# Kernel optimization log

Measured on AMD Instinct MI355X. Metric: run time of the kernel, lower is better.

The kernel has to match this reference:

```python
import jax, jax.numpy as jnp
import numpy as np

NUM_HEADS = 8


def _ln(x, w, b, eps=1e-5):
    mu = x.mean(-1, keepdims=True)
    var = ((x - mu) ** 2).mean(-1, keepdims=True)
    return (x - mu) * jax.lax.rsqrt(var + eps) * w + b


def _qkv(x, w, H, d):
    # x: (n, l, C) -> q,k,v each (n, H, l, d)
    n, l, _ = x.shape
    qkv = (x @ w.T).reshape(n, l, 3, H, d)
    qkv = jnp.transpose(qkv, (2, 0, 3, 1, 4))
    return qkv[0], qkv[1], qkv[2]


def _qkv_head(x, w, d):
    # x: (n, H, l, d) -> q,k,v each (n, H, l, d); linear acts on head_dim
    n, H, l, _ = x.shape
    qkv = (x @ w.T).reshape(n, H, l, 3, d)
    qkv = jnp.transpose(qkv, (3, 0, 1, 2, 4))
    return qkv[0], qkv[1], qkv[2]


def _attn(q, k, v, scale):
    s = jax.nn.softmax(jnp.einsum('nhqd,nhkd->nhqk', q, k) * scale, axis=-1)
    return jnp.einsum('nhqk,nhkd->nhqd', s, v)


def setup_inputs() -> dict:
    key = jax.random.key(0)
    ks = jax.random.split(key, 10)
    B, N, C = 16, 4096, 512
    l = 64
    H, d = NUM_HEADS, C // NUM_HEADS
    return {
        'x': jax.random.normal(ks[0], (B, N, C), jnp.float32),
        'n3_w': jnp.ones((C,), jnp.float32),
        'n3_b': jnp.zeros((C,), jnp.float32),
        'n4_w': jnp.ones((C,), jnp.float32),
        'n4_b': jnp.zeros((C,), jnp.float32),
        'ln1_w': jax.random.normal(ks[1], (3 * C, C), jnp.float32) * 0.02,
        'ln2_w': jax.random.normal(ks[2], (3 * C, C), jnp.float32) * 0.02,
        'ln3_w': jax.random.normal(ks[3], (3 * d, d), jnp.float32) * 0.02,
        'ln4_w': jax.random.normal(ks[4], (3 * d, d), jnp.float32) * 0.02,
        'pos1': jax.random.normal(ks[5], (1, l, C), jnp.float32),
        'pos2': jax.random.normal(ks[6], (1, l, C), jnp.float32),
        'pos3': jax.random.normal(ks[7], (1, H, l, d), jnp.float32),
        'pos4': jax.random.normal(ks[8], (1, H, l, d), jnp.float32),
    }


def reference(x, n3_w, n3_b, n4_w, n4_b, ln1_w, ln2_w, ln3_w, ln4_w,
              pos1, pos2, pos3, pos4):
    B, N, C = x.shape
    l = int(np.sqrt(N))
    H = NUM_HEADS
    d = C // H
    scale = d ** -0.5

    # window (row) branch
    x_w = _ln(x, n3_w, n3_b).reshape(B * l, l, C) + pos1
    q, k, v = _qkv(x_w, ln1_w, H, d)
    x_ww = _attn(q, k, v, scale) + pos3                     # (B*l, H, l, d)
    xw_q, xw_k, xw_v = _qkv_head(x_ww, ln3_w, d)

    # height (column) branch: transpose the l x l grid
    x_h = _ln(x, n4_w, n4_b).reshape(B, l, l, C)
    x_h = jnp.swapaxes(x_h, 1, 2).reshape(B * l, l, C) + pos2
    q, k, v = _qkv(x_h, ln2_w, H, d)
    x_hh = _attn(q, k, v, scale) + pos4
    xh_q, xh_k, xh_v = _qkv_head(x_hh, ln4_w, d)

    # cross-attention between the two axial branches
    o1 = _attn(xh_q, xw_k, xw_v, scale)                     # (B*l, H, l, d)
    o1 = jnp.swapaxes(o1, 1, 2).reshape(B, l, l, C)
    o1 = jnp.swapaxes(o1, 1, 2)
    o2 = _attn(xw_q, xh_k, xh_v, scale)
    o2 = jnp.swapaxes(o2, 1, 2).reshape(B, l, l, C)

    out = (o1 + o2).reshape(B, N, C) + x
    return out
```

## Files before the change

kernel.cpp:

```cpp
#include <hip/hip_runtime.h>

typedef unsigned short u16;
typedef __attribute__((ext_vector_type(8))) short bf16x8;
typedef __attribute__((ext_vector_type(4))) float floatx4;
typedef __attribute__((ext_vector_type(4))) unsigned short u16x4;

__device__ __forceinline__ float b2f(u16 u) {
  unsigned int i = ((unsigned int)u) << 16;
  return __builtin_bit_cast(float, i);
}
__device__ __forceinline__ u16 f2b(float f) {
  unsigned int i = __builtin_bit_cast(unsigned int, f);
  i += 0x7fffu + ((i >> 16) & 1u);
  return (u16)(i >> 16);
}
#define MFMA16(a, b, c) __builtin_amdgcn_mfma_f32_16x16x32_bf16((a), (b), (c), 0, 0, 0)
#define LGKM0() __asm__ volatile("s_waitcnt lgkmcnt(0)" ::: "memory")

__device__ __forceinline__ void gload_lds16(const u16* g, u16* l) {
  __builtin_amdgcn_global_load_lds(
      (const __attribute__((address_space(1))) void*)g,
      (__attribute__((address_space(3))) void*)l, 16, 0, 0);
}

__global__ __launch_bounds__(256) void cvt_kernel(const float* __restrict__ a,
                                                  u16* __restrict__ o, int n4) {
  int i = blockIdx.x * 256 + threadIdx.x;
  if (i < n4) {
    float4 v = ((const float4*)a)[i];
    u16x4 r;
    r.x = f2b(v.x); r.y = f2b(v.y); r.z = f2b(v.z); r.w = f2b(v.w);
    ((u16x4*)o)[i] = r;
  }
}

__global__ __launch_bounds__(256) void ln_pos_kernel(
    const float* __restrict__ x, const float* __restrict__ n3w, const float* __restrict__ n3b,
    const float* __restrict__ n4w, const float* __restrict__ n4b,
    const float* __restrict__ pos1, const float* __restrict__ pos2,
    u16* __restrict__ yW, u16* __restrict__ yH) {
  int wv = threadIdx.x >> 6, lane = threadIdx.x & 63;
  int token = blockIdx.x * 4 + wv;
  int b = token >> 12, r = (token >> 6) & 63, c = token & 63;
  const float4* xr = (const float4*)(x + (size_t)token * 512) + lane * 2;
  float4 x0 = xr[0], x1 = xr[1];
  float v[8] = {x0.x, x0.y, x0.z, x0.w, x1.x, x1.y, x1.z, x1.w};
  float s = 0.f, ss = 0.f;
#pragma unroll
  for (int j = 0; j < 8; j++) { s += v[j]; ss += v[j] * v[j]; }
#pragma unroll
  for (int off = 1; off < 64; off <<= 1) { s += __shfl_xor(s, off); ss += __shfl_xor(ss, off); }
  float mu = s * (1.0f / 512.0f);
  float var = ss * (1.0f / 512.0f) - mu * mu;
  float rs = rsqrtf(var + 1e-5f);
  int ch0 = lane * 8;
  float w3[8], b3[8], w4[8], b4[8], p1[8], p2[8];
  *(float4*)&w3[0] = *(const float4*)(n3w + ch0); *(float4*)&w3[4] = *(const float4*)(n3w + ch0 + 4);
  *(float4*)&b3[0] = *(const float4*)(n3b + ch0); *(float4*)&b3[4] = *(const float4*)(n3b + ch0 + 4);
  *(float4*)&w4[0] = *(const float4*)(n4w + ch0); *(float4*)&w4[4] = *(const float4*)(n4w + ch0 + 4);
  *(float4*)&b4[0] = *(const float4*)(n4b + ch0); *(float4*)&b4[4] = *(const float4*)(n4b + ch0 + 4);
  const float* p1p = pos1 + (size_t)c * 512 + ch0;
  const float* p2p = pos2 + (size_t)r * 512 + ch0;
  *(float4*)&p1[0] = *(const float4*)p1p; *(float4*)&p1[4] = *(const float4*)(p1p + 4);
  *(float4*)&p2[0] = *(const float4*)p2p; *(float4*)&p2[4] = *(const float4*)(p2p + 4);
  bf16x8 ow, oh;
#pragma unroll
  for (int j = 0; j < 8; j++) {
    float xn = (v[j] - mu) * rs;
    ow[j] = (short)f2b(xn * w3[j] + b3[j] + p1[j]);
    oh[j] = (short)f2b(xn * w4[j] + b4[j] + p2[j]);
  }
  *(bf16x8*)(yW + (size_t)token * 512 + ch0) = ow;
  size_t hrow = (size_t)b * 4096 + (size_t)c * 64 + r;
  *(bf16x8*)(yH + hrow * 512 + ch0) = oh;
}

__global__ __launch_bounds__(256) void qkv_gemm_kernel(
    const u16* __restrict__ A0, const u16* __restrict__ A1,
    const u16* __restrict__ W0, const u16* __restrict__ W1,
    u16* __restrict__ Z0, u16* __restrict__ Z1) {
  const int K = 512, N = 1536;
  int br = blockIdx.z;
  const u16* A = br ? A1 : A0;
  const u16* W = br ? W1 : W0;
  u16* Z = br ? Z1 : Z0;
  int n0 = blockIdx.x * 128, m0 = blockIdx.y * 128;
  __shared__ u16 gpool[8192];
  u16 (*As)[32] = (u16(*)[32])gpool;
  u16 (*Bs)[32] = (u16(*)[32])(gpool + 4096);
  int tid = threadIdx.x, lane = tid & 63, wave = tid >> 6;
  int wm = (wave >> 1) * 64, wn = (wave & 1) * 64;
  int ml = lane & 15, quad = lane >> 4;
  floatx4 acc[4][4];
#pragma unroll
  for (int mi = 0; mi < 4; mi++)
#pragma unroll
    for (int ni = 0; ni < 4; ni++) acc[mi][ni] = (floatx4){0.f, 0.f, 0.f, 0.f};

  int srow = (lane >> 2);
  int scol = (lane & 3) * 8;
  for (int kt = 0; kt < K; kt += 32) {
#pragma unroll
    for (int i = 0; i < 2; i++) {
      int rbase = wave * 32 + i * 16;
      gload_lds16(A + (size_t)(m0 + rbase + srow) * K + kt + scol, &As[rbase][0]);
      gload_lds16(W + (size_t)(n0 + rbase + srow) * K + kt + scol, &Bs[rbase][0]);
    }
    __syncthreads();
    bf16x8 a[4], bfr[4];
#pragma unroll
    for (int mi = 0; mi < 4; mi++) a[mi] = *(const bf16x8*)&As[wm + mi * 16 + ml][quad * 8];
#pragma unroll
    for (int ni = 0; ni < 4; ni++) bfr[ni] = *(const bf16x8*)&Bs[wn + ni * 16 + ml][quad * 8];
#pragma unroll
    for (int mi = 0; mi < 4; mi++)
#pragma unroll
      for (int ni = 0; ni < 4; ni++) acc[mi][ni] = MFMA16(a[mi], bfr[ni], acc[mi][ni]);
    __syncthreads();
  }
  u16* wl = gpool + wave * 2048;
#pragma unroll
  for (int pair = 0; pair < 2; pair++) {
#pragma unroll
    for (int mh = 0; mh < 2; mh++) {
      int mi = pair * 2 + mh;
#pragma unroll
      for (int ni = 0; ni < 4; ni++)
#pragma unroll
        for (int r = 0; r < 4; r++)
          wl[(mh * 16 + quad * 4 + r) * 64 + ni * 16 + ml] = f2b(acc[mi][ni][r]);
    }
    LGKM0();
#pragma unroll
    for (int p = 0; p < 4; p++) {
      int lrow = p * 8 + (lane >> 3);
      int col8 = (lane & 7) * 8;
      bf16x8 vv = *(const bf16x8*)&wl[lrow * 64 + col8];
      int rg = m0 + wm + pair * 32 + lrow;
      *(bf16x8*)&Z[(size_t)rg * N + n0 + wn + col8] = vv;
    }
    LGKM0();
  }
}

__device__ __forceinline__ void attn_core(bf16x8 aq0, bf16x8 aq1,
                                          const u16 (*Ks)[72], const u16 (*Vt)[72],
                                          u16 (*Psw)[72], int lane, floatx4 o[4]) {
  int ml = lane & 15, quad = lane >> 4;
  floatx4 s[4];
#pragma unroll
  for (int nt = 0; nt < 4; nt++) {
    floatx4 z = (floatx4){0.f, 0.f, 0.f, 0.f};
    bf16x8 b0 = *(const bf16x8*)&Ks[nt * 16 + ml][quad * 8];
    bf16x8 b1 = *(const bf16x8*)&Ks[nt * 16 + ml][32 + quad * 8];
    z = MFMA16(aq0, b0, z);
    z = MFMA16(aq1, b1, z);
    s[nt] = z;
  }
#pragma unroll
  for (int r = 0; r < 4; r++) {
    float m = -1e30f;
#pragma unroll
    for (int nt = 0; nt < 4; nt++) { s[nt][r] *= 0.125f; m = fmaxf(m, s[nt][r]); }
#pragma unroll
    for (int off = 1; off < 16; off <<= 1) m = fmaxf(m, __shfl_xor(m, off));
    float su = 0.f;
#pragma unroll
    for (int nt = 0; nt < 4; nt++) { float p = __expf(s[nt][r] - m); s[nt][r] = p; su += p; }
#pragma unroll
    for (int off = 1; off < 16; off <<= 1) su += __shfl_xor(su, off);
    float inv = 1.0f / su;
#pragma unroll
    for (int nt = 0; nt < 4; nt++) s[nt][r] *= inv;
  }
#pragma unroll
  for (int nt = 0; nt < 4; nt++)
#pragma unroll
    for (int r = 0; r < 4; r++) Psw[quad * 4 + r][nt * 16 + ml] = f2b(s[nt][r]);
  LGKM0();
  bf16x8 ap0 = *(const bf16x8*)&Psw[ml][quad * 8];
  bf16x8 ap1 = *(const bf16x8*)&Psw[ml][32 + quad * 8];
#pragma unroll
  for (int et = 0; et < 4; et++) {
    floatx4 z = (floatx4){0.f, 0.f, 0.f, 0.f};
    bf16x8 b0 = *(const bf16x8*)&Vt[et * 16 + ml][quad * 8];
    bf16x8 b1 = *(const bf16x8*)&Vt[et * 16 + ml][32 + quad * 8];
    z = MFMA16(ap0, b0, z);
    z = MFMA16(ap1, b1, z);
    o[et] = z;
  }
}

__device__ __forceinline__ void head_qkv(const floatx4 o[4], const float* pp,
                                         const u16* lw, u16 (*Ks)[72], u16 (*Vt)[72],
                                         u16 (*Ps)[72], int wv, int lane,
                                         bf16x8& axq0, bf16x8& axq1) {
  int ml = lane & 15, quad = lane >> 4;
#pragma unroll
  for (int et = 0; et < 4; et++)
#pragma unroll
    for (int r = 0; r < 4; r++) {
      int qp = wv * 16 + quad * 4 + r, e = et * 16 + ml;
      Ps[quad * 4 + r][et * 16 + ml] = f2b(o[et][r] + pp[(size_t)qp * 64 + e]);
    }
  LGKM0();
  bf16x8 ax0 = *(const bf16x8*)&Ps[ml][quad * 8];
  bf16x8 ax1 = *(const bf16x8*)&Ps[ml][32 + quad * 8];
  LGKM0();
  __builtin_amdgcn_sched_barrier(0);
#pragma unroll
  for (int nj = 0; nj < 4; nj++) {
    int col = 64 + nj * 16 + ml;
    bf16x8 b0 = *(const bf16x8*)(lw + (size_t)col * 64 + quad * 8);
    bf16x8 b1 = *(const bf16x8*)(lw + (size_t)col * 64 + 32 + quad * 8);
    floatx4 z = (floatx4){0.f, 0.f, 0.f, 0.f};
    z = MFMA16(ax0, b0, z);
    z = MFMA16(ax1, b1, z);
#pragma unroll
    for (int r = 0; r < 4; r++)
      Ks[wv * 16 + quad * 4 + r][nj * 16 + ml] = f2b(z[r]);
  }
#pragma unroll
  for (int nj = 0; nj < 4; nj++) {
    int col = 128 + nj * 16 + ml;
    bf16x8 b0 = *(const bf16x8*)(lw + (size_t)col * 64 + quad * 8);
    bf16x8 b1 = *(const bf16x8*)(lw + (size_t)col * 64 + 32 + quad * 8);
    floatx4 z = (floatx4){0.f, 0.f, 0.f, 0.f};
    z = MFMA16(ax0, b0, z);
    z = MFMA16(ax1, b1, z);
#pragma unroll
    for (int r = 0; r < 4; r++)
      Vt[nj * 16 + ml][wv * 16 + quad * 4 + r] = f2b(z[r]);
  }
#pragma unroll
  for (int nj = 0; nj < 4; nj++) {
    int col = nj * 16 + ml;
    bf16x8 b0 = *(const bf16x8*)(lw + (size_t)col * 64 + quad * 8);
    bf16x8 b1 = *(const bf16x8*)(lw + (size_t)col * 64 + 32 + quad * 8);
    floatx4 z = (floatx4){0.f, 0.f, 0.f, 0.f};
    z = MFMA16(ax0, b0, z);
    z = MFMA16(ax1, b1, z);
#pragma unroll
    for (int r = 0; r < 4; r++)
      Ps[quad * 4 + r][nj * 16 + ml] = f2b(z[r]);
  }
  LGKM0();
  __builtin_amdgcn_sched_barrier(0);
  axq0 = *(const bf16x8*)&Ps[ml][quad * 8];
  axq1 = *(const bf16x8*)&Ps[ml][32 + quad * 8];
  LGKM0();
}

__global__ __launch_bounds__(256) void fused_attn_kernel(
    const u16* __restrict__ Zw, const u16* __restrict__ Zh,
    const u16* __restrict__ l3b, const u16* __restrict__ l4b,
    const float* __restrict__ pos3, const float* __restrict__ pos4,
    u16* __restrict__ o1b, u16* __restrict__ o2b) {
  int w = blockIdx.x, h = blockIdx.y;
  __shared__ u16 pool[23040];
  u16 (*KsW)[72] = (u16(*)[72])pool;
  u16 (*VtW)[72] = (u16(*)[72])(pool + 4608);
  u16 (*KsH)[72] = (u16(*)[72])(pool + 9216);
  u16 (*VtH)[72] = (u16(*)[72])(pool + 13824);
  int tid = threadIdx.x, lane = tid & 63, wv = tid >> 6;
  int ml = lane & 15, quad = lane >> 4;
  u16 (*Ps)[72] = (u16(*)[72])(pool + 18432 + wv * 1152);
  const u16* baseW = Zw + (size_t)w * 64 * 1536 + h * 64;
  const u16* baseH = Zh + (size_t)w * 64 * 1536 + h * 64;
  for (int i = tid; i < 512; i += 256) {
    int r = i >> 3, c = (i & 7) * 8;
    *(bf16x8*)&KsW[r][c] = *(const bf16x8*)(baseW + 512 + (size_t)r * 1536 + c);
    *(bf16x8*)&KsH[r][c] = *(const bf16x8*)(baseH + 512 + (size_t)r * 1536 + c);
  }
  for (int i = tid; i < 1024; i += 256) {
    int p = i >> 4, e0 = (i & 15) * 4;
    u16x4 vW = *(const u16x4*)(baseW + 1024 + (size_t)p * 1536 + e0);
    u16x4 vH = *(const u16x4*)(baseH + 1024 + (size_t)p * 1536 + e0);
    VtW[e0 + 0][p] = vW.x; VtW[e0 + 1][p] = vW.y; VtW[e0 + 2][p] = vW.z; VtW[e0 + 3][p] = vW.w;
    VtH[e0 + 0][p] = vH.x; VtH[e0 + 1][p] = vH.y; VtH[e0 + 2][p] = vH.z; VtH[e0 + 3][p] = vH.w;
  }
  const u16* qrW = baseW + (size_t)(wv * 16 + ml) * 1536 + quad * 8;
  const u16* qrH = baseH + (size_t)(wv * 16 + ml) * 1536 + quad * 8;
  bf16x8 aqW0 = *(const bf16x8*)qrW;
  bf16x8 aqW1 = *(const bf16x8*)(qrW + 32);
  bf16x8 aqH0 = *(const bf16x8*)qrH;
  bf16x8 aqH1 = *(const bf16x8*)(qrH + 32);
  __syncthreads();
  floatx4 oW[4], oH[4];
  attn_core(aqW0, aqW1, KsW, VtW, Ps, lane, oW);
  attn_core(aqH0, aqH1, KsH, VtH, Ps, lane, oH);
  __syncthreads();
  bf16x8 axqW0, axqW1, axqH0, axqH1;
  head_qkv(oW, pos3 + (size_t)h * 4096, l3b, KsW, VtW, Ps, wv, lane, axqW0, axqW1);
  __syncthreads();
  head_qkv(oH, pos4 + (size_t)h * 4096, l4b, KsH, VtH, Ps, wv, lane, axqH0, axqH1);
  __syncthreads();
  floatx4 c2[4], c1[4];
  attn_core(axqW0, axqW1, KsH, VtH, Ps, lane, c2);
  attn_core(axqH0, axqH1, KsW, VtW, Ps, lane, c1);
  __syncthreads();
  u16* Out1 = pool;
  u16* Out2 = pool + 4608;
#pragma unroll
  for (int et = 0; et < 4; et++)
#pragma unroll
    for (int r = 0; r < 4; r++) {
      int row = wv * 16 + quad * 4 + r;
      Out1[row * 64 + et * 16 + ml] = f2b(c1[et][r]);
      Out2[row * 64 + et * 16 + ml] = f2b(c2[et][r]);
    }
  __syncthreads();
  u16* o1p = o1b + (size_t)w * 32768 + h * 64;
  u16* o2p = o2b + (size_t)w * 32768 + h * 64;
#pragma unroll
  for (int j = 0; j < 2; j++) {
    int c = tid + j * 256;
    int pos = c >> 3, cc = (c & 7) * 8;
    *(bf16x8*)&o1p[(size_t)pos * 512 + cc] = *(const bf16x8*)&Out1[pos * 64 + cc];
    *(bf16x8*)&o2p[(size_t)pos * 512 + cc] = *(const bf16x8*)&Out2[pos * 64 + cc];
  }
}

__global__ __launch_bounds__(256) void final_add_kernel(
    const float* __restrict__ x, const u16* __restrict__ o1b,
    const u16* __restrict__ o2b, float* __restrict__ out) {
  int wv = threadIdx.x >> 6, lane = threadIdx.x & 63;
  int token = blockIdx.x * 4 + wv;
  int b = token >> 12, r = (token >> 6) & 63, c = token & 63;
  size_t i = (size_t)token * 512 + lane * 8;
  size_t i1 = ((size_t)b * 4096 + (size_t)c * 64 + r) * 512 + lane * 8;
  float vx[8];
  *(float4*)&vx[0] = *(const float4*)(x + i);
  *(float4*)&vx[4] = *(const float4*)(x + i + 4);
  bf16x8 v1 = *(const bf16x8*)(o1b + i1);
  bf16x8 v2 = *(const bf16x8*)(o2b + i);
  float vo[8];
#pragma unroll
  for (int j = 0; j < 8; j++)
    vo[j] = vx[j] + b2f((u16)v1[j]) + b2f((u16)v2[j]);
  *(float4*)(out + i) = *(float4*)&vo[0];
  *(float4*)(out + i + 4) = *(float4*)&vo[4];
}

extern "C" void kernel_launch(void* const* d_in, const int* in_sizes, int n_in,
                              void* d_out, int out_size, void* d_ws, size_t ws_size,
                              hipStream_t stream) {
  const float* x    = (const float*)d_in[0];
  const float* n3w  = (const float*)d_in[1];
  const float* n3b  = (const float*)d_in[2];
  const float* n4w  = (const float*)d_in[3];
  const float* n4b  = (const float*)d_in[4];
  const float* ln1  = (const float*)d_in[5];
  const float* ln2  = (const float*)d_in[6];
  const float* ln3  = (const float*)d_in[7];
  const float* ln4  = (const float*)d_in[8];
  const float* pos1 = (const float*)d_in[9];
  const float* pos2 = (const float*)d_in[10];
  const float* pos3 = (const float*)d_in[11];
  const float* pos4 = (const float*)d_in[12];

  char* ws = (char*)d_ws;
  u16* yW = (u16*)ws;
  u16* yH = (u16*)(ws + (size_t)67108864);
  u16* Zw = (u16*)(ws + (size_t)134217728);
  u16* Zh = (u16*)(ws + (size_t)335544320);
  u16* o1b = yW;
  u16* o2b = yH;
  float* out = (float*)d_out;

  u16* Wb1 = (u16*)d_out;
  u16* Wb2 = Wb1 + 786432;
  u16* l3b = Wb2 + 786432;
  u16* l4b = l3b + 12288;

  cvt_kernel<<<768, 256, 0, stream>>>(ln1, Wb1, 196608);
  cvt_kernel<<<768, 256, 0, stream>>>(ln2, Wb2, 196608);
  cvt_kernel<<<12, 256, 0, stream>>>(ln3, l3b, 3072);
  cvt_kernel<<<12, 256, 0, stream>>>(ln4, l4b, 3072);
  ln_pos_kernel<<<16384, 256, 0, stream>>>(x, n3w, n3b, n4w, n4b, pos1, pos2, yW, yH);
  qkv_gemm_kernel<<<dim3(12, 512, 2), 256, 0, stream>>>(yW, yH, Wb1, Wb2, Zw, Zh);
  fused_attn_kernel<<<dim3(1024, 8), 256, 0, stream>>>(Zw, Zh, l3b, l4b, pos3, pos4, o1b, o2b);
  final_add_kernel<<<16384, 256, 0, stream>>>(x, o1b, o2b, out);
}
```

Before: 915.4 us.

## Double-buffer QKV GEMM LDS tiles and remap blocks for L2 locality

The QKV projection GEMM now double-buffers its A/W tiles in LDS, so the global_load_lds for the next K-slice is issued before the MFMAs on the current slice run. This is meant to hide global memory latency behind compute. It also remaps the block index so that consecutive blocks are spread across M tiles in a way meant to improve L2 reuse. The cost is twice the LDS per block, which may lower occupancy, plus an explicit vmcnt wait each iteration.

```diff
diff --git a/kernel.cpp b/kernel.cpp
--- a/kernel.cpp
+++ b/kernel.cpp
@@ -16,6 +16,7 @@
 }
 #define MFMA16(a, b, c) __builtin_amdgcn_mfma_f32_16x16x32_bf16((a), (b), (c), 0, 0, 0)
 #define LGKM0() __asm__ volatile("s_waitcnt lgkmcnt(0)" ::: "memory")
+#define VM0() __asm__ volatile("s_waitcnt vmcnt(0)" ::: "memory")
 
 __device__ __forceinline__ void gload_lds16(const u16* g, u16* l) {
   __builtin_amdgcn_global_load_lds(
@@ -84,10 +85,10 @@
   const u16* A = br ? A1 : A0;
   const u16* W = br ? W1 : W0;
   u16* Z = br ? Z1 : Z0;
-  int n0 = blockIdx.x * 128, m0 = blockIdx.y * 128;
-  __shared__ u16 gpool[8192];
-  u16 (*As)[32] = (u16(*)[32])gpool;
-  u16 (*Bs)[32] = (u16(*)[32])(gpool + 4096);
+  int lin = blockIdx.y * 12 + blockIdx.x;
+  int nl = (lin & 7) * 768 + (lin >> 3);
+  int n0 = (nl % 12) * 128, m0 = (nl / 12) * 128;
+  __shared__ u16 gpool[16384];
   int tid = threadIdx.x, lane = tid & 63, wave = tid >> 6;
   int wm = (wave >> 1) * 64, wn = (wave & 1) * 64;
   int ml = lane & 15, quad = lane >> 4;
@@ -99,23 +100,44 @@
 
   int srow = (lane >> 2);
   int scol = (lane & 3) * 8;
-  for (int kt = 0; kt < K; kt += 32) {
+  {
+    u16 (*As)[32] = (u16(*)[32])gpool;
+    u16 (*Bs)[32] = (u16(*)[32])(gpool + 4096);
 #pragma unroll
     for (int i = 0; i < 2; i++) {
       int rbase = wave * 32 + i * 16;
-      gload_lds16(A + (size_t)(m0 + rbase + srow) * K + kt + scol, &As[rbase][0]);
-      gload_lds16(W + (size_t)(n0 + rbase + srow) * K + kt + scol, &Bs[rbase][0]);
-    }
-    __syncthreads();
+      gload_lds16(A + (size_t)(m0 + rbase + srow) * K + scol, &As[rbase][0]);
+      gload_lds16(W + (size_t)(n0 + rbase + srow) * K + scol, &Bs[rbase][0]);
+    }
+  }
+  VM0();
+  __syncthreads();
+  for (int t = 0; t < 16; ++t) {
+    u16* cb = gpool + (t & 1) * 8192;
+    u16* nb = gpool + ((t & 1) ^ 1) * 8192;
+    if (t < 15) {
+      int kt = (t + 1) * 32;
+      u16 (*As)[32] = (u16(*)[32])nb;
+      u16 (*Bs)[32] = (u16(*)[32])(nb + 4096);
+#pragma unroll
+      for (int i = 0; i < 2; i++) {
+        int rbase = wave * 32 + i * 16;
+        gload_lds16(A + (size_t)(m0 + rbase + srow) * K + kt + scol, &As[rbase][0]);
+        gload_lds16(W + (size_t)(n0 + rbase + srow) * K + kt + scol, &Bs[rbase][0]);
+      }
+    }
+    u16 (*Asc)[32] = (u16(*)[32])cb;
+    u16 (*Bsc)[32] = (u16(*)[32])(cb + 4096);
     bf16x8 a[4], bfr[4];
 #pragma unroll
-    for (int mi = 0; mi < 4; mi++) a[mi] = *(const bf16x8*)&As[wm + mi * 16 + ml][quad * 8];
-#pragma unroll
-    for (int ni = 0; ni < 4; ni++) bfr[ni] = *(const bf16x8*)&Bs[wn + ni * 16 + ml][quad * 8];
+    for (int mi = 0; mi < 4; mi++) a[mi] = *(const bf16x8*)&Asc[wm + mi * 16 + ml][quad * 8];
+#pragma unroll
+    for (int ni = 0; ni < 4; ni++) bfr[ni] = *(const bf16x8*)&Bsc[wn + ni * 16 + ml][quad * 8];
 #pragma unroll
     for (int mi = 0; mi < 4; mi++)
 #pragma unroll
       for (int ni = 0; ni < 4; ni++) acc[mi][ni] = MFMA16(a[mi], bfr[ni], acc[mi][ni]);
+    VM0();
     __syncthreads();
   }
   u16* wl = gpool + wave * 2048;
```

New measurement: 898.2 us. About the same (-1.9%).
